# Kernel tuning notes

Measured on AMD Instinct MI355X. Metric: run time of the kernel, lower is better.

The kernel has to match this reference:

```python
import jax, jax.numpy as jnp
import numpy as np

B, T, E = 2, 2048, 768
H = 12
HD = E // H          # 64
ROT = 32             # rotary dim (= head_dim // 2 in CLVP)
SCALE = HD ** -0.5


def rotate_half(x):
    # split last dim into (2, d/2), rotate second half by 90 deg
    x = x.reshape(*x.shape[:-1], 2, x.shape[-1] // 2)
    x1, x2 = x[..., 0, :], x[..., 1, :]
    return jnp.concatenate([-x2, x1], axis=-1)


def apply_rotary_pos_emb(state, freqs):
    # state: (B*H, T, HD); freqs: (1, T, ROT)
    pos_emb_len = freqs.shape[-1]
    s_l, s_r = state[..., :pos_emb_len], state[..., pos_emb_len:]
    f = freqs[:, :, -s_l.shape[-1]:]
    s_l = s_l * jnp.cos(f) + rotate_half(s_l) * jnp.sin(f)
    return jnp.concatenate([s_l, s_r], axis=-1)


def setup_inputs() -> dict:
    key = jax.random.key(0)
    ks = jax.random.split(key, 6)
    hidden_states = jax.random.normal(ks[0], (B, T, E), dtype=jnp.float32)
    rotary_pos_emb = jax.random.uniform(ks[1], (1, T, ROT), dtype=jnp.float32)
    Wq = jax.random.normal(ks[2], (E, E), dtype=jnp.float32) * 0.02
    Wk = jax.random.normal(ks[3], (E, E), dtype=jnp.float32) * 0.02
    Wv = jax.random.normal(ks[4], (E, E), dtype=jnp.float32) * 0.02
    Wo = jax.random.normal(ks[5], (E, E), dtype=jnp.float32) * 0.02
    bo = jnp.zeros((E,), dtype=jnp.float32)
    return {"hidden_states": hidden_states, "rotary_pos_emb": rotary_pos_emb,
            "Wq": Wq, "Wk": Wk, "Wv": Wv, "Wo": Wo, "bo": bo}


def _shape(x):
    # (B, T, E) -> (B*H, T, HD)
    return x.reshape(B, T, H, HD).transpose(0, 2, 1, 3).reshape(B * H, T, HD)


def reference(hidden_states, rotary_pos_emb, Wq, Wk, Wv, Wo, bo):
    # nn.Linear: x @ W.T
    q = _shape(hidden_states @ Wq.T * SCALE)
    k = _shape(hidden_states @ Wk.T)
    v = _shape(hidden_states @ Wv.T)

    q = apply_rotary_pos_emb(q, rotary_pos_emb)
    k = apply_rotary_pos_emb(k, rotary_pos_emb)
    v = apply_rotary_pos_emb(v, rotary_pos_emb)  # CLVP applies RoPE to V too

    attn = jax.nn.softmax(jnp.einsum('bqd,bkd->bqk', q, k), axis=-1)  # (B*H, T, T)
    out = jnp.einsum('bqk,bkd->bqd', attn, v)                          # (B*H, T, HD)
    out = out.reshape(B, H, T, HD).transpose(0, 2, 1, 3).reshape(B, T, E)
    return out @ Wo.T + bo
```

## Files before the change

kernel.cpp:

```cpp
#include <hip/hip_runtime.h>
#include <hip/hip_bf16.h>

typedef unsigned short ushort_t;
typedef __attribute__((ext_vector_type(8))) short short8;
typedef __attribute__((ext_vector_type(4))) float f32x4;

constexpr int B  = 2;
constexpr int T  = 2048;
constexpr int E  = 768;
constexpr int H  = 12;
constexpr int HD = 64;

__device__ __forceinline__ ushort_t f2bf(float x) {
  unsigned int u = __float_as_uint(x);
  u += 0x7fffu + ((u >> 16) & 1u);
  return (ushort_t)(u >> 16);
}

__device__ __forceinline__ unsigned int pack_bf2(float a, float b) {
  __hip_bfloat162 h = __float22bfloat162_rn(float2{a, b});
  return *(unsigned int*)&h;
}

__device__ __forceinline__ int swz(int row, int col) {
  return row * 64 + ((((col >> 3) ^ (row & 7)) << 3) | (col & 7));
}

__global__ __launch_bounds__(256) void cvt_all(
    const float* __restrict__ X,  const float* __restrict__ Wq,
    const float* __restrict__ Wk, const float* __restrict__ Wv,
    const float* __restrict__ Wo, const float* __restrict__ rope,
    ushort_t* __restrict__ Xb,  ushort_t* __restrict__ Wqb,
    ushort_t* __restrict__ Wkb, ushort_t* __restrict__ Wvb,
    ushort_t* __restrict__ Wob, float* __restrict__ ct, float* __restrict__ st)
{
  constexpr int NX4 = (B * T * E) / 4;
  constexpr int NW4 = (E * E) / 4;
  constexpr int NC4 = NX4 + 4 * NW4;
  int i = blockIdx.x * 256 + threadIdx.x;
  if (i < NC4) {
    const float* s; ushort_t* d; int j;
    if (i < NX4) { s = X; d = Xb; j = i; }
    else {
      int t = i - NX4;
      int w = t / NW4; j = t - w * NW4;
      s = (w == 0) ? Wq : (w == 1) ? Wk : (w == 2) ? Wv : Wo;
      d = (w == 0) ? Wqb : (w == 1) ? Wkb : (w == 2) ? Wvb : Wob;
    }
    float4 v = ((const float4*)s)[j];
    ushort4 o;
    o.x = f2bf(v.x); o.y = f2bf(v.y); o.z = f2bf(v.z); o.w = f2bf(v.w);
    ((ushort4*)d)[j] = o;
  } else {
    int j = (i - NC4) * 4;
    float4 f = *(const float4*)(rope + j);
    float c, s;
    sincosf(f.x, &s, &c); ct[j+0] = c; st[j+0] = s;
    sincosf(f.y, &s, &c); ct[j+1] = c; st[j+1] = s;
    sincosf(f.z, &s, &c); ct[j+2] = c; st[j+2] = s;
    sincosf(f.w, &s, &c); ct[j+3] = c; st[j+3] = s;
  }
}

__global__ __launch_bounds__(256) void qkv_gemm(
    const ushort_t* __restrict__ Xb,
    const ushort_t* __restrict__ Wqb, const ushort_t* __restrict__ Wkb,
    const ushort_t* __restrict__ Wvb,
    const float* __restrict__ ct, const float* __restrict__ st,
    ushort_t* __restrict__ qfb, ushort_t* __restrict__ kfb, ushort_t* __restrict__ vfb)
{
  __shared__ __align__(16) ushort_t smem[128 * 64 + 64 * 64];
  ushort_t* Xs = smem;
  ushort_t* Ws = smem + 128 * 64;
  const int tid  = threadIdx.x;
  const int wave = tid >> 6;
  const int lane = tid & 63;
  const int l15  = lane & 15, quad = lane >> 4;
  const int n0 = blockIdx.x * 64;
  const int m0 = blockIdx.y * 128;
  const int z  = blockIdx.z;
  const ushort_t* Wt = (z == 0) ? Wqb : (z == 1) ? Wkb : Wvb;
  const int h = n0 >> 6;

  f32x4 acc[2][4];
  #pragma unroll
  for (int i = 0; i < 2; ++i)
    #pragma unroll
    for (int j = 0; j < 4; ++j) acc[i][j] = (f32x4){0.f, 0.f, 0.f, 0.f};

  const int srX = tid >> 1, scX = (tid & 1) * 32;
  const int srW = tid >> 2, scW = (tid & 3) * 16;

  for (int k0 = 0; k0 < E; k0 += 64) {
    uint4 x0 = *(const uint4*)(Xb + (size_t)(m0 + srX) * E + k0 + scX);
    uint4 x1 = *(const uint4*)(Xb + (size_t)(m0 + srX) * E + k0 + scX + 8);
    uint4 x2 = *(const uint4*)(Xb + (size_t)(m0 + srX) * E + k0 + scX + 16);
    uint4 x3 = *(const uint4*)(Xb + (size_t)(m0 + srX) * E + k0 + scX + 24);
    uint4 w0 = *(const uint4*)(Wt + (size_t)(n0 + srW) * E + k0 + scW);
    uint4 w1 = *(const uint4*)(Wt + (size_t)(n0 + srW) * E + k0 + scW + 8);
    *(uint4*)&Xs[swz(srX, scX)]      = x0;
    *(uint4*)&Xs[swz(srX, scX + 8)]  = x1;
    *(uint4*)&Xs[swz(srX, scX + 16)] = x2;
    *(uint4*)&Xs[swz(srX, scX + 24)] = x3;
    *(uint4*)&Ws[swz(srW, scW)]      = w0;
    *(uint4*)&Ws[swz(srW, scW + 8)]  = w1;
    __syncthreads();
    short8 a[2][2];
    #pragma unroll
    for (int mt = 0; mt < 2; ++mt)
      #pragma unroll
      for (int kh = 0; kh < 2; ++kh)
        a[mt][kh] = *(const short8*)&Xs[swz(wave * 32 + mt * 16 + l15, kh * 32 + quad * 8)];
    #pragma unroll
    for (int nt = 0; nt < 4; ++nt) {
      #pragma unroll
      for (int kh = 0; kh < 2; ++kh) {
        short8 bb = *(const short8*)&Ws[swz(nt * 16 + l15, kh * 32 + quad * 8)];
        #pragma unroll
        for (int mt = 0; mt < 2; ++mt)
          acc[mt][nt] = __builtin_amdgcn_mfma_f32_16x16x32_bf16(a[mt][kh], bb, acc[mt][nt], 0, 0, 0);
      }
    }
    __syncthreads();
  }

  const int b  = m0 >> 11;
  const int t0 = m0 & (T - 1);
  const int bh = b * H + h;
  const float qscale = (z == 0) ? 0.125f : 1.0f;

  if (z < 2) {
    #pragma unroll
    for (int mt = 0; mt < 2; ++mt) {
      #pragma unroll
      for (int r = 0; r < 4; ++r) {
        int mloc = wave * 32 + mt * 16 + quad * 4 + r;
        int t = (m0 + mloc) & (T - 1);
        float s0 = acc[mt][0][r] * qscale;
        float s1 = acc[mt][1][r] * qscale;
        float c0v = ct[t * 32 + l15],      sn0 = st[t * 32 + l15];
        float c1v = ct[t * 32 + 16 + l15], sn1 = st[t * 32 + 16 + l15];
        smem[swz(mloc, l15)]      = f2bf(s0 * c0v - s1 * sn0);
        smem[swz(mloc, 16 + l15)] = f2bf(s1 * c1v + s0 * sn1);
        smem[swz(mloc, 32 + l15)] = f2bf(acc[mt][2][r] * qscale);
        smem[swz(mloc, 48 + l15)] = f2bf(acc[mt][3][r] * qscale);
      }
    }
    __syncthreads();
    if (z == 0) {
      #pragma unroll
      for (int i = 0; i < 4; ++i) {
        int p = tid + 256 * i;
        int qtl = p >> 7, kh = (p >> 6) & 1, ln = p & 63;
        int tl = qtl * 16 + (ln & 15);
        int d  = kh * 32 + (ln >> 4) * 8;
        uint4 v = *(const uint4*)&smem[swz(tl, d)];
        size_t off = ((size_t)((bh * 128 + (t0 >> 4) + qtl) * 2 + kh)) * 512 + ln * 8;
        *(uint4*)(qfb + off) = v;
      }
    } else {
      #pragma unroll
      for (int i = 0; i < 4; ++i) {
        int p = tid + 256 * i;
        int ktl = p >> 9, mt = (p >> 7) & 3, kh = (p >> 6) & 1, ln = p & 63;
        int tl = ktl * 64 + mt * 16 + (ln & 15);
        int d  = kh * 32 + (ln >> 4) * 8;
        uint4 v = *(const uint4*)&smem[swz(tl, d)];
        size_t off = ((size_t)(((bh * 32 + (t0 >> 6) + ktl) * 4 + mt) * 2 + kh)) * 512 + ln * 8;
        *(uint4*)(kfb + off) = v;
      }
    }
  } else {
    #pragma unroll
    for (int mt = 0; mt < 2; ++mt) {
      #pragma unroll
      for (int r = 0; r < 4; ++r) {
        int mloc = wave * 32 + mt * 16 + quad * 4 + r;
        int t = (m0 + mloc) & (T - 1);
        float s0 = acc[mt][0][r], s1 = acc[mt][1][r];
        float c0v = ct[t * 32 + l15],      sn0 = st[t * 32 + l15];
        float c1v = ct[t * 32 + 16 + l15], sn1 = st[t * 32 + 16 + l15];
        smem[(l15)      * 132 + mloc] = f2bf(s0 * c0v - s1 * sn0);
        smem[(16 + l15) * 132 + mloc] = f2bf(s1 * c1v + s0 * sn1);
        smem[(32 + l15) * 132 + mloc] = f2bf(acc[mt][2][r]);
        smem[(48 + l15) * 132 + mloc] = f2bf(acc[mt][3][r]);
      }
    }
    __syncthreads();
    #pragma unroll
    for (int i = 0; i < 4; ++i) {
      int p = tid + 256 * i;
      int ktl = p >> 9, nt = (p >> 7) & 3, kh = (p >> 6) & 1, ln = p & 63;
      int d  = nt * 16 + (ln & 15);
      int tl = ktl * 64 + kh * 32 + (ln >> 4) * 8;
      uint4 v = *(const uint4*)&smem[d * 132 + tl];
      size_t off = ((size_t)(((bh * 32 + (t0 >> 6) + ktl) * 4 + nt) * 2 + kh)) * 512 + ln * 8;
      *(uint4*)(vfb + off) = v;
    }
  }
}

__global__ __launch_bounds__(256, 5) void attn_kernel(
    const ushort_t* __restrict__ qfb, const ushort_t* __restrict__ kfb,
    const ushort_t* __restrict__ vfb, ushort_t* __restrict__ cbuf)
{
  __shared__ __align__(16) ushort_t Ps[4][16 * 64];
  __shared__ __align__(16) float Osh[4][16][68];
  __shared__ float Lsh[4][16];
  const int tid  = threadIdx.x;
  const int wave = tid >> 6;
  const int lane = tid & 63;
  const int l15  = lane & 15, quad = lane >> 4;
  const int qg = blockIdx.x;
  const int bh = blockIdx.y;
  const ushort_t* Qf = qfb + (size_t)bh * (T * HD);
  const ushort_t* Kf = kfb + (size_t)bh * (T * HD);
  const ushort_t* Vf = vfb + (size_t)bh * (T * HD);
  ushort_t* Pw = &Ps[wave][0];

  short8 qa[2];
  #pragma unroll
  for (int kh = 0; kh < 2; ++kh)
    qa[kh] = *(const short8*)(Qf + ((size_t)(qg * 2 + kh)) * 512 + lane * 8);

  f32x4 o[4];
  #pragma unroll
  for (int nt = 0; nt < 4; ++nt) o[nt] = (f32x4){0.f, 0.f, 0.f, 0.f};
  float lsum = 0.f;

  for (int kt = wave; kt < T / 64; kt += 4) {
    short8 ka[4][2], va[4][2];
    #pragma unroll
    for (int mt = 0; mt < 4; ++mt)
      #pragma unroll
      for (int kh = 0; kh < 2; ++kh) {
        ka[mt][kh] = *(const short8*)(Kf + ((size_t)((kt * 4 + mt) * 2 + kh)) * 512 + lane * 8);
        va[mt][kh] = *(const short8*)(Vf + ((size_t)((kt * 4 + mt) * 2 + kh)) * 512 + lane * 8);
      }

    f32x4 ss[4];
    #pragma unroll
    for (int mt = 0; mt < 4; ++mt) ss[mt] = (f32x4){0.f, 0.f, 0.f, 0.f};
    #pragma unroll
    for (int mt = 0; mt < 4; ++mt) {
      ss[mt] = __builtin_amdgcn_mfma_f32_16x16x32_bf16(ka[mt][0], qa[0], ss[mt], 0, 0, 0);
      ss[mt] = __builtin_amdgcn_mfma_f32_16x16x32_bf16(ka[mt][1], qa[1], ss[mt], 0, 0, 0);
    }

    #pragma unroll
    for (int mt = 0; mt < 4; ++mt) {
      float p0 = __expf(ss[mt][0]);
      float p1 = __expf(ss[mt][1]);
      float p2 = __expf(ss[mt][2]);
      float p3 = __expf(ss[mt][3]);
      lsum += (p0 + p1) + (p2 + p3);
      uint2 w2;
      w2.x = pack_bf2(p0, p1);
      w2.y = pack_bf2(p2, p3);
      *(uint2*)&Pw[swz(l15, mt * 16 + quad * 4)] = w2;
    }

    short8 pa0 = *(const short8*)&Pw[swz(l15, quad * 8)];
    short8 pa1 = *(const short8*)&Pw[swz(l15, 32 + quad * 8)];
    #pragma unroll
    for (int nt = 0; nt < 4; ++nt) {
      o[nt] = __builtin_amdgcn_mfma_f32_16x16x32_bf16(pa0, va[nt][0], o[nt], 0, 0, 0);
      o[nt] = __builtin_amdgcn_mfma_f32_16x16x32_bf16(pa1, va[nt][1], o[nt], 0, 0, 0);
    }
  }

  lsum += __shfl_xor(lsum, 16);
  lsum += __shfl_xor(lsum, 32);
  if (lane < 16) Lsh[wave][l15] = lsum;

  #pragma unroll
  for (int nt = 0; nt < 4; ++nt)
    #pragma unroll
    for (int r = 0; r < 4; ++r)
      Osh[wave][quad * 4 + r][nt * 16 + l15] = o[nt][r];
  __syncthreads();

  const int row = tid >> 4;
  const int c4  = (tid & 15) * 4;
  float4 s = *(const float4*)&Osh[0][row][c4];
  #pragma unroll
  for (int w = 1; w < 4; ++w) {
    float4 t = *(const float4*)&Osh[w][row][c4];
    s.x += t.x; s.y += t.y; s.z += t.z; s.w += t.w;
  }
  float inv = 1.0f / (Lsh[0][row] + Lsh[1][row] + Lsh[2][row] + Lsh[3][row]);
  const int b = bh / H, h = bh % H;
  int t = qg * 16 + row;
  size_t base = ((size_t)b * T + t) * E + h * HD + c4;
  uint2 w2;
  w2.x = pack_bf2(s.x * inv, s.y * inv);
  w2.y = pack_bf2(s.z * inv, s.w * inv);
  *(uint2*)(cbuf + base) = w2;
}

__global__ __launch_bounds__(256) void out_gemm(
    const ushort_t* __restrict__ Xc, const ushort_t* __restrict__ Wob,
    const float* __restrict__ bo, float* __restrict__ out)
{
  __shared__ __align__(16) ushort_t Xs[128 * 64];
  __shared__ __align__(16) ushort_t Ws[64 * 64];
  const int tid  = threadIdx.x;
  const int wave = tid >> 6;
  const int lane = tid & 63;
  const int l15  = lane & 15, quad = lane >> 4;
  const int n0 = blockIdx.x * 64;
  const int m0 = blockIdx.y * 128;

  f32x4 acc[2][4];
  #pragma unroll
  for (int i = 0; i < 2; ++i)
    #pragma unroll
    for (int j = 0; j < 4; ++j) acc[i][j] = (f32x4){0.f, 0.f, 0.f, 0.f};

  const int srX = tid >> 1, scX = (tid & 1) * 32;
  const int srW = tid >> 2, scW = (tid & 3) * 16;

  for (int k0 = 0; k0 < E; k0 += 64) {
    uint4 x0 = *(const uint4*)(Xc + (size_t)(m0 + srX) * E + k0 + scX);
    uint4 x1 = *(const uint4*)(Xc + (size_t)(m0 + srX) * E + k0 + scX + 8);
    uint4 x2 = *(const uint4*)(Xc + (size_t)(m0 + srX) * E + k0 + scX + 16);
    uint4 x3 = *(const uint4*)(Xc + (size_t)(m0 + srX) * E + k0 + scX + 24);
    uint4 w0 = *(const uint4*)(Wob + (size_t)(n0 + srW) * E + k0 + scW);
    uint4 w1 = *(const uint4*)(Wob + (size_t)(n0 + srW) * E + k0 + scW + 8);
    *(uint4*)&Xs[swz(srX, scX)]      = x0;
    *(uint4*)&Xs[swz(srX, scX + 8)]  = x1;
    *(uint4*)&Xs[swz(srX, scX + 16)] = x2;
    *(uint4*)&Xs[swz(srX, scX + 24)] = x3;
    *(uint4*)&Ws[swz(srW, scW)]      = w0;
    *(uint4*)&Ws[swz(srW, scW + 8)]  = w1;
    __syncthreads();
    short8 a[2][2];
    #pragma unroll
    for (int mt = 0; mt < 2; ++mt)
      #pragma unroll
      for (int kh = 0; kh < 2; ++kh)
        a[mt][kh] = *(const short8*)&Xs[swz(wave * 32 + mt * 16 + l15, kh * 32 + quad * 8)];
    #pragma unroll
    for (int nt = 0; nt < 4; ++nt) {
      #pragma unroll
      for (int kh = 0; kh < 2; ++kh) {
        short8 bb = *(const short8*)&Ws[swz(nt * 16 + l15, kh * 32 + quad * 8)];
        #pragma unroll
        for (int mt = 0; mt < 2; ++mt)
          acc[mt][nt] = __builtin_amdgcn_mfma_f32_16x16x32_bf16(a[mt][kh], bb, acc[mt][nt], 0, 0, 0);
      }
    }
    __syncthreads();
  }

  float bias[4];
  #pragma unroll
  for (int nt = 0; nt < 4; ++nt) bias[nt] = bo[n0 + nt * 16 + l15];
  #pragma unroll
  for (int mt = 0; mt < 2; ++mt) {
    #pragma unroll
    for (int r = 0; r < 4; ++r) {
      int m = m0 + wave * 32 + mt * 16 + quad * 4 + r;
      float* op = out + (size_t)m * E + n0;
      op[l15]      = acc[mt][0][r] + bias[0];
      op[16 + l15] = acc[mt][1][r] + bias[1];
      op[32 + l15] = acc[mt][2][r] + bias[2];
      op[48 + l15] = acc[mt][3][r] + bias[3];
    }
  }
}

extern "C" void kernel_launch(void* const* d_in, const int* in_sizes, int n_in,
                              void* d_out, int out_size, void* d_ws, size_t ws_size,
                              hipStream_t stream) {
  (void)in_sizes; (void)n_in; (void)out_size; (void)ws_size;
  const float* X    = (const float*)d_in[0];
  const float* rope = (const float*)d_in[1];
  const float* Wq   = (const float*)d_in[2];
  const float* Wk   = (const float*)d_in[3];
  const float* Wv   = (const float*)d_in[4];
  const float* Wo   = (const float*)d_in[5];
  const float* bo   = (const float*)d_in[6];
  float* out = (float*)d_out;

  const size_t NX = (size_t)B * T * E;
  const size_t NW = (size_t)E * E;
  const size_t NR = (size_t)T * 32;
  ushort_t* Xb  = (ushort_t*)d_ws;
  ushort_t* Wqb = Xb  + NX;
  ushort_t* Wkb = Wqb + NW;
  ushort_t* Wvb = Wkb + NW;
  ushort_t* Wob = Wvb + NW;
  ushort_t* qfb = Wob + NW;
  ushort_t* kfb = qfb + NX;
  ushort_t* vfb = kfb + NX;
  ushort_t* cb  = vfb + NX;
  float* ct = (float*)(cb + NX);
  float* st = ct + NR;

  const int total4 = (int)((NX + 4 * NW + NR) / 4);
  cvt_all<<<total4 / 256, 256, 0, stream>>>(X, Wq, Wk, Wv, Wo, rope,
                                            Xb, Wqb, Wkb, Wvb, Wob, ct, st);

  qkv_gemm<<<dim3(E / 64, (B * T) / 128, 3), 256, 0, stream>>>(
      Xb, Wqb, Wkb, Wvb, ct, st, qfb, kfb, vfb);
  attn_kernel<<<dim3(T / 16, B * H), 256, 0, stream>>>(qfb, kfb, vfb, cb);
  out_gemm<<<dim3(E / 64, (B * T) / 128), 256, 0, stream>>>(cb, Wob, bo, out);
}
```

Before: 185.5 us.

## Enlarge attention query tile to 64 rows with 2x2 wave split and K/V prefetch

```diff
diff --git a/kernel.cpp b/kernel.cpp
--- a/kernel.cpp
+++ b/kernel.cpp
@@ -200,102 +200,143 @@
   }
 }
 
-__global__ __launch_bounds__(256, 5) void attn_kernel(
+__global__ __launch_bounds__(256) void attn_kernel(
     const ushort_t* __restrict__ qfb, const ushort_t* __restrict__ kfb,
     const ushort_t* __restrict__ vfb, ushort_t* __restrict__ cbuf)
 {
-  __shared__ __align__(16) ushort_t Ps[4][16 * 64];
-  __shared__ __align__(16) float Osh[4][16][68];
-  __shared__ float Lsh[4][16];
+  __shared__ __align__(16) ushort_t Ps[4][32 * 40];
+  __shared__ __align__(16) float Osh[2][32][66];
+  __shared__ float Lsh[2][32];
   const int tid  = threadIdx.x;
   const int wave = tid >> 6;
+  const int wq = wave >> 1, wk = wave & 1;
   const int lane = tid & 63;
   const int l15  = lane & 15, quad = lane >> 4;
-  const int qg = blockIdx.x;
+  const int q0 = blockIdx.x * 64;
   const int bh = blockIdx.y;
   const ushort_t* Qf = qfb + (size_t)bh * (T * HD);
   const ushort_t* Kf = kfb + (size_t)bh * (T * HD);
   const ushort_t* Vf = vfb + (size_t)bh * (T * HD);
   ushort_t* Pw = &Ps[wave][0];
 
-  short8 qa[2];
-  #pragma unroll
-  for (int kh = 0; kh < 2; ++kh)
-    qa[kh] = *(const short8*)(Qf + ((size_t)(qg * 2 + kh)) * 512 + lane * 8);
-
-  f32x4 o[4];
-  #pragma unroll
-  for (int nt = 0; nt < 4; ++nt) o[nt] = (f32x4){0.f, 0.f, 0.f, 0.f};
-  float lsum = 0.f;
-
-  for (int kt = wave; kt < T / 64; kt += 4) {
-    short8 ka[4][2], va[4][2];
-    #pragma unroll
-    for (int mt = 0; mt < 4; ++mt)
-      #pragma unroll
-      for (int kh = 0; kh < 2; ++kh) {
-        ka[mt][kh] = *(const short8*)(Kf + ((size_t)((kt * 4 + mt) * 2 + kh)) * 512 + lane * 8);
-        va[mt][kh] = *(const short8*)(Vf + ((size_t)((kt * 4 + mt) * 2 + kh)) * 512 + lane * 8);
-      }
-
-    f32x4 ss[4];
-    #pragma unroll
-    for (int mt = 0; mt < 4; ++mt) ss[mt] = (f32x4){0.f, 0.f, 0.f, 0.f};
-    #pragma unroll
-    for (int mt = 0; mt < 4; ++mt) {
-      ss[mt] = __builtin_amdgcn_mfma_f32_16x16x32_bf16(ka[mt][0], qa[0], ss[mt], 0, 0, 0);
-      ss[mt] = __builtin_amdgcn_mfma_f32_16x16x32_bf16(ka[mt][1], qa[1], ss[mt], 0, 0, 0);
-    }
-
-    #pragma unroll
-    for (int mt = 0; mt < 4; ++mt) {
-      float p0 = __expf(ss[mt][0]);
-      float p1 = __expf(ss[mt][1]);
-      float p2 = __expf(ss[mt][2]);
-      float p3 = __expf(ss[mt][3]);
-      lsum += (p0 + p1) + (p2 + p3);
-      uint2 w2;
-      w2.x = pack_bf2(p0, p1);
-      w2.y = pack_bf2(p2, p3);
-      *(uint2*)&Pw[swz(l15, mt * 16 + quad * 4)] = w2;
-    }
-
-    short8 pa0 = *(const short8*)&Pw[swz(l15, quad * 8)];
-    short8 pa1 = *(const short8*)&Pw[swz(l15, 32 + quad * 8)];
+  short8 qa[2][2];
+  #pragma unroll
+  for (int qg = 0; qg < 2; ++qg)
+    #pragma unroll
+    for (int kh = 0; kh < 2; ++kh)
+      qa[qg][kh] = *(const short8*)(Qf + ((size_t)(((q0 >> 4) + wq * 2 + qg) * 2 + kh)) * 512 + lane * 8);
+
+  short8 ka[2][2], va[4];
+  #pragma unroll
+  for (int i = 0; i < 2; ++i)
+    #pragma unroll
+    for (int kh = 0; kh < 2; ++kh)
+      ka[i][kh] = *(const short8*)(Kf + ((size_t)((wk * 2 + i) * 2 + kh)) * 512 + lane * 8);
+  #pragma unroll
+  for (int nt = 0; nt < 4; ++nt)
+    va[nt] = *(const short8*)(Vf + ((size_t)(nt * 2 + wk)) * 512 + lane * 8);
+
+  f32x4 o[2][4];
+  #pragma unroll
+  for (int qg = 0; qg < 2; ++qg)
+    #pragma unroll
+    for (int nt = 0; nt < 4; ++nt) o[qg][nt] = (f32x4){0.f, 0.f, 0.f, 0.f};
+  float lsum[2] = {0.f, 0.f};
+
+  for (int kt = 0; kt < T / 64; ++kt) {
+    const int ktn = (kt + 1 < T / 64) ? kt + 1 : kt;
+    short8 kn[2][2], vn[4];
+    #pragma unroll
+    for (int i = 0; i < 2; ++i)
+      #pragma unroll
+      for (int kh = 0; kh < 2; ++kh)
+        kn[i][kh] = *(const short8*)(Kf + ((size_t)((ktn * 4 + wk * 2 + i) * 2 + kh)) * 512 + lane * 8);
+    #pragma unroll
+    for (int nt = 0; nt < 4; ++nt)
+      vn[nt] = *(const short8*)(Vf + ((size_t)((ktn * 4 + nt) * 2 + wk)) * 512 + lane * 8);
+
+    f32x4 ss[2][2];
+    #pragma unroll
+    for (int mt = 0; mt < 2; ++mt)
+      #pragma unroll
+      for (int qg = 0; qg < 2; ++qg) {
+        ss[mt][qg] = (f32x4){0.f, 0.f, 0.f, 0.f};
+        ss[mt][qg] = __builtin_amdgcn_mfma_f32_16x16x32_bf16(ka[mt][0], qa[qg][0], ss[mt][qg], 0, 0, 0);
+        ss[mt][qg] = __builtin_amdgcn_mfma_f32_16x16x32_bf16(ka[mt][1], qa[qg][1], ss[mt][qg], 0, 0, 0);
+      }
+
+    #pragma unroll
+    for (int qg = 0; qg < 2; ++qg) {
+      #pragma unroll
+      for (int mt = 0; mt < 2; ++mt) {
+        float p0 = __expf(ss[mt][qg][0]);
+        float p1 = __expf(ss[mt][qg][1]);
+        float p2 = __expf(ss[mt][qg][2]);
+        float p3 = __expf(ss[mt][qg][3]);
+        lsum[qg] += (p0 + p1) + (p2 + p3);
+        uint2 w2;
+        w2.x = pack_bf2(p0, p1);
+        w2.y = pack_bf2(p2, p3);
+        *(uint2*)&Pw[(qg * 16 + l15) * 40 + mt * 16 + quad * 4] = w2;
+      }
+    }
+
+    short8 pa0 = *(const short8*)&Pw[(l15) * 40 + quad * 8];
+    short8 pa1 = *(const short8*)&Pw[(16 + l15) * 40 + quad * 8];
     #pragma unroll
     for (int nt = 0; nt < 4; ++nt) {
-      o[nt] = __builtin_amdgcn_mfma_f32_16x16x32_bf16(pa0, va[nt][0], o[nt], 0, 0, 0);
-      o[nt] = __builtin_amdgcn_mfma_f32_16x16x32_bf16(pa1, va[nt][1], o[nt], 0, 0, 0);
-    }
-  }
-
-  lsum += __shfl_xor(lsum, 16);
-  lsum += __shfl_xor(lsum, 32);
-  if (lane < 16) Lsh[wave][l15] = lsum;
-
-  #pragma unroll
-  for (int nt = 0; nt < 4; ++nt)
-    #pragma unroll
-    for (int r = 0; r < 4; ++r)
-      Osh[wave][quad * 4 + r][nt * 16 + l15] = o[nt][r];
+      o[0][nt] = __builtin_amdgcn_mfma_f32_16x16x32_bf16(pa0, va[nt], o[0][nt], 0, 0, 0);
+      o[1][nt] = __builtin_amdgcn_mfma_f32_16x16x32_bf16(pa1, va[nt], o[1][nt], 0, 0, 0);
+    }
+
+    #pragma unroll
+    for (int i = 0; i < 2; ++i) {
+      ka[i][0] = kn[i][0];
+      ka[i][1] = kn[i][1];
+    }
+    #pragma unroll
+    for (int nt = 0; nt < 4; ++nt) va[nt] = vn[nt];
+  }
+
+  #pragma unroll
+  for (int qg = 0; qg < 2; ++qg) {
+    lsum[qg] += __shfl_xor(lsum[qg], 16);
+    lsum[qg] += __shfl_xor(lsum[qg], 32);
+  }
+
+  if (wk == 0) {
+    #pragma unroll
+    for (int qg = 0; qg < 2; ++qg)
+      #pragma unroll
+      for (int nt = 0; nt < 4; ++nt)
+        #pragma unroll
+        for (int r = 0; r < 4; ++r)
+          Osh[wq][qg * 16 + quad * 4 + r][nt * 16 + l15] = o[qg][nt][r];
+    if (lane < 16) {
+      Lsh[wq][l15]      = lsum[0];
+      Lsh[wq][16 + l15] = lsum[1];
+    }
+  }
   __syncthreads();
-
-  const int row = tid >> 4;
-  const int c4  = (tid & 15) * 4;
-  float4 s = *(const float4*)&Osh[0][row][c4];
-  #pragma unroll
-  for (int w = 1; w < 4; ++w) {
-    float4 t = *(const float4*)&Osh[w][row][c4];
-    s.x += t.x; s.y += t.y; s.z += t.z; s.w += t.w;
-  }
-  float inv = 1.0f / (Lsh[0][row] + Lsh[1][row] + Lsh[2][row] + Lsh[3][row]);
-  const int b = bh / H, h = bh % H;
-  int t = qg * 16 + row;
-  size_t base = ((size_t)b * T + t) * E + h * HD + c4;
-  uint2 w2;
-  w2.x = pack_bf2(s.x * inv, s.y * inv);
-  w2.y = pack_bf2(s.z * inv, s.w * inv);
-  *(uint2*)(cbuf + base) = w2;
+  if (wk == 1) {
+    const int b = bh / H, h = bh % H;
+    #pragma unroll
+    for (int qg = 0; qg < 2; ++qg) {
+      float ltot = lsum[qg] + Lsh[wq][qg * 16 + l15];
+      float inv0 = 1.0f / ltot;
+      #pragma unroll
+      for (int r = 0; r < 4; ++r) {
+        float inv = __shfl(inv0, quad * 4 + r);
+        int t = q0 + wq * 32 + qg * 16 + quad * 4 + r;
+        size_t base = ((size_t)b * T + t) * E + h * HD;
+        #pragma unroll
+        for (int nt = 0; nt < 4; ++nt) {
+          float v = o[qg][nt][r] + Osh[wq][qg * 16 + quad * 4 + r][nt * 16 + l15];
+          cbuf[base + nt * 16 + l15] = f2bf(v * inv);
+        }
+      }
+    }
+  }
 }
 
 __global__ __launch_bounds__(256) void out_gemm(
@@ -404,6 +445,6 @@
 
   qkv_gemm<<<dim3(E / 64, (B * T) / 128, 3), 256, 0, stream>>>(
       Xb, Wqb, Wkb, Wvb, ct, st, qfb, kfb, vfb);
-  attn_kernel<<<dim3(T / 16, B * H), 256, 0, stream>>>(qfb, kfb, vfb, cb);
+  attn_kernel<<<dim3(T / 64, B * H), 256, 0, stream>>>(qfb, kfb, vfb, cb);
   out_gemm<<<dim3(E / 64, (B * T) / 128), 256, 0, stream>>>(cb, Wob, bo, out);
 }
```

Measured after the change: 166.2 us. 10.4% less time.
